# Kernel tuning notes

Hardware: AMD Instinct MI355X
Metric: run time of the kernel (lower is better)

Reference implementation:

```python
import jax, jax.numpy as jnp
import numpy as np


@jax.custom_vjp
def binary_act(x):
    # sign forward, straight-through (clipped) backward, matching BinaryActivation
    return jnp.sign(x)

def _ba_fwd(x):
    return jnp.sign(x), x

def _ba_bwd(x, g):
    return (jnp.where((x >= -1.0) & (x <= 1.0), g, 0.0),)

binary_act.defvjp(_ba_fwd, _ba_bwd)


def conv2d(x, w, b, pad, groups):
    # x: NCHW, w: OIHW
    y = jax.lax.conv_general_dilated(
        x, w, window_strides=(1, 1), padding=[(pad, pad), (pad, pad)],
        feature_group_count=groups,
        dimension_numbers=("NCHW", "OIHW", "NCHW"))
    return y + b[None, :, None, None]


def bconv(x, w, b, pad, groups):
    # Binary_conv2d: weights and bias binarized via sign (no STE on weights in torch either)
    return conv2d(x, jnp.sign(w), jnp.sign(b), pad, groups)


def maxpool2(x):
    return jax.lax.reduce_window(x, -jnp.inf, jax.lax.max,
                                 (1, 1, 2, 2), (1, 1, 2, 2), "VALID")


def setup_inputs() -> dict:
    key = jax.random.key(0)
    ks = jax.random.split(key, 14)
    d = {}
    d["x"] = jax.random.normal(ks[0], (1024, 3, 32, 32), dtype=jnp.float32)
    # conv1: depthwise 3x3 (groups=3) then 1x1 3->128
    d["w1_dw"] = jax.random.normal(ks[1], (3, 1, 3, 3), dtype=jnp.float32) * 0.1
    d["b1_dw"] = jax.random.normal(ks[2], (3,), dtype=jnp.float32) * 0.1
    d["w1_pw"] = jax.random.normal(ks[3], (128, 3, 1, 1), dtype=jnp.float32) * 0.1
    d["b1_pw"] = jax.random.normal(ks[4], (128,), dtype=jnp.float32) * 0.1
    # conv2: depthwise 3x3 (groups=128) then 1x1 128->256
    d["w2_dw"] = jax.random.normal(ks[5], (128, 1, 3, 3), dtype=jnp.float32) * 0.1
    d["b2_dw"] = jax.random.normal(ks[6], (128,), dtype=jnp.float32) * 0.1
    d["w2_pw"] = jax.random.normal(ks[7], (256, 128, 1, 1), dtype=jnp.float32) * 0.1
    d["b2_pw"] = jax.random.normal(ks[8], (256,), dtype=jnp.float32) * 0.1
    # fc layers (full precision weights, sign applied to fc1 output only)
    d["fc1_w"] = jax.random.normal(ks[9], (1024, 256 * 8 * 8), dtype=jnp.float32) * (1.0 / np.sqrt(256 * 8 * 8))
    d["fc1_b"] = jnp.zeros((1024,), dtype=jnp.float32)
    d["fc2_w"] = jax.random.normal(ks[10], (10, 1024), dtype=jnp.float32) * (1.0 / np.sqrt(1024.0))
    d["fc2_b"] = jnp.zeros((10,), dtype=jnp.float32)
    return d


def reference(x, w1_dw, b1_dw, w1_pw, b1_pw, w2_dw, b2_dw, w2_pw, b2_pw,
              fc1_w, fc1_b, fc2_w, fc2_b):
    h = bconv(x, w1_dw, b1_dw, pad=1, groups=3)        # [B,3,32,32]
    h = bconv(h, w1_pw, b1_pw, pad=0, groups=1)        # [B,128,32,32]
    h = maxpool2(binary_act(h))                        # [B,128,16,16]
    h = bconv(h, w2_dw, b2_dw, pad=1, groups=128)      # [B,128,16,16]
    h = bconv(h, w2_pw, b2_pw, pad=0, groups=1)        # [B,256,16,16]
    h = maxpool2(binary_act(h))                        # [B,256,8,8]
    h = h.reshape(h.shape[0], -1)                      # [B,16384]
    h = binary_act(h @ fc1_w.T + fc1_b)                # [B,1024]
    return h @ fc2_w.T + fc2_b                         # [B,10]
```

## Files before the change

kernel.cpp:

```cpp
#include <hip/hip_runtime.h>


__device__ __forceinline__ int fsign(float v)  { return (v > 0.f) - (v < 0.f); }
__device__ __forceinline__ int dsign(double v) { return (v > 0.0) - (v < 0.0); }

typedef int v4i __attribute__((ext_vector_type(4)));

__device__ __forceinline__ void async16(const signed char* g, signed char* l) {
    __builtin_amdgcn_global_load_lds(
        (const __attribute__((address_space(1))) void*)g,
        (__attribute__((address_space(3))) void*)l, 16, 0, 0);
}

__global__ void k1_conv1(const float* __restrict__ x,
                         const float* __restrict__ w1dw, const float* __restrict__ b1dw,
                         const float* __restrict__ w1pw, const float* __restrict__ b1pw,
                         signed char* __restrict__ pooled1T)
{
    __shared__ float sdw[27], sbdw[3];
    __shared__ unsigned char spidx[128];
    int t = threadIdx.x;
    if (t < 27) sdw[t] = (float)fsign(w1dw[t]);
    if (t < 3)  sbdw[t] = (float)fsign(b1dw[t]);
    if (t < 128) {
        int b0 = w1pw[t * 3 + 0] > 0.f;
        int b1 = w1pw[t * 3 + 1] > 0.f;
        int b2 = w1pw[t * 3 + 2] > 0.f;
        int b3 = b1pw[t] > 0.f;
        spidx[t] = (unsigned char)(b0 | (b1 << 1) | (b2 << 2) | (b3 << 3));
    }
    __syncthreads();

    int g  = blockIdx.x * 256 + t;
    int px = g & 15, py = (g >> 4) & 15, n = g >> 8;

    double h[3][4];
    const float* xb = x + (size_t)n * 3 * 1024;
    #pragma unroll
    for (int c = 0; c < 3; c++) {
        const float* xc = xb + c * 1024;
        #pragma unroll
        for (int dy = 0; dy < 2; dy++)
        #pragma unroll
        for (int dx = 0; dx < 2; dx++) {
            int y = 2 * py + dy, xx = 2 * px + dx;
            double acc = (double)sbdw[c];
            #pragma unroll
            for (int ky = 0; ky < 3; ky++) {
                int yy = y + ky - 1;
                if (yy < 0 || yy > 31) continue;
                #pragma unroll
                for (int kx = 0; kx < 3; kx++) {
                    int xxx = xx + kx - 1;
                    if (xxx < 0 || xxx > 31) continue;
                    acc += (double)sdw[c * 9 + ky * 3 + kx] * (double)xc[yy * 32 + xxx];
                }
            }
            h[c][dy * 2 + dx] = acc;
        }
    }

    double tv[4][4];
    #pragma unroll
    for (int q = 0; q < 4; q++) {
        double u = h[0][q] + h[1][q];
        double v = h[0][q] - h[1][q];
        tv[0][q] = v - h[2][q];
        tv[1][q] = u - h[2][q];
        tv[2][q] = v + h[2][q];
        tv[3][q] = u + h[2][q];
    }
    int mpack = 0;
    #pragma unroll
    for (int bp = 0; bp < 4; bp++) {
        int mxP = -2, mnP = 2, mxM = -2, mnM = 2;
        #pragma unroll
        for (int q = 0; q < 4; q++) {
            int sP = dsign(tv[bp][q] + 1.0);
            int sM = dsign(tv[bp][q] - 1.0);
            mxP = max(mxP, sP); mnP = min(mnP, sP);
            mxM = max(mxM, sM); mnM = min(mnM, sM);
        }
        int pat1 = 1 | (bp << 1);
        int pat0 = (~pat1) & 7;
        mpack |= (mxP + 1)   << (2 * (pat1 | 8));
        mpack |= (mxM + 1)   << (2 * pat1);
        mpack |= ((-mnM) + 1) << (2 * (pat0 | 8));
        mpack |= ((-mnP) + 1) << (2 * pat0);
    }

    signed char* outb = pooled1T + (size_t)n * 32768 + (py * 16 + px) * 128;
    const int* pint = (const int*)spidx;
    for (int ob = 0; ob < 32; ob++) {
        int pw = pint[ob];
        int cur = 0;
        #pragma unroll
        for (int e = 0; e < 4; e++) {
            int pi = (pw >> (8 * e)) & 15;
            int mv = ((mpack >> (pi * 2)) & 3) - 1;
            cur |= (mv & 0xff) << (8 * e);
        }
        *(int*)(outb + ob * 4) = cur;
    }
}

__global__ void kprep2(const float* __restrict__ w2pw, const float* __restrict__ b2pw,
                       signed char* __restrict__ w2s, int* __restrict__ b2adj)
{
    int o = blockIdx.x * 64 + threadIdx.x;
    int rs = 0;
    for (int cq = 0; cq < 32; cq++) {
        float4 w = *(const float4*)(w2pw + (size_t)o * 128 + cq * 4);
        int s0 = fsign(w.x), s1 = fsign(w.y), s2 = fsign(w.z), s3 = fsign(w.w);
        rs += s0 + s1 + s2 + s3;
        int pk = (s0 & 0xff) | ((s1 & 0xff) << 8) | ((s2 & 0xff) << 16) | ((s3 & 0xff) << 24);
        *(int*)(w2s + (size_t)o * 128 + cq * 4) = pk;
    }
    b2adj[o] = fsign(b2pw[o]) - 32 * rs;
}

__global__ __launch_bounds__(256, 3) void k3_fused(
    const signed char* __restrict__ pooled1T,
    const float* __restrict__ w2dw, const float* __restrict__ b2dw,
    const signed char* __restrict__ w2s, const int* __restrict__ b2adj,
    signed char* __restrict__ hT2)
{
    __shared__ __align__(16) signed char Ps[32768];
    __shared__ __align__(16) signed char sw4[1152];
    __shared__ __align__(16) signed char sdb2[128];
    __shared__ int sb2adj[256];
    __shared__ __align__(16) signed char Os[64 * 80];

    int t = threadIdx.x, l = t & 63, wid = t >> 6;
    int n = blockIdx.x;
    const signed char* pb = pooled1T + (size_t)n * 32768;

    #pragma unroll
    for (int it = 0; it < 8; it++) {
        int off = it * 4096 + t * 16;
        int p = off >> 7, seg = (off >> 4) & 7;
        *(int4*)&Ps[p * 128 + ((seg ^ (p & 7)) * 16)] = *(const int4*)(pb + off);
    }
    for (int i = t; i < 1152; i += 256) {
        int c = i & 127, tap = i >> 7;
        sw4[tap * 128 + c] = (signed char)fsign(w2dw[c * 9 + tap]);
    }
    if (t < 128) sdb2[t] = (signed char)(fsign(b2dw[t]) + 1);
    if (t < 256) sb2adj[t] = b2adj[t];
    __syncthreads();

    int frow = l & 15;

    v4i af[4][2];
    #pragma unroll
    for (int ks = 0; ks < 2; ks++) {
        int c0 = ks * 64 + (l >> 4) * 16;
        int cc = c0 >> 4;
        int4 w4[9];
        #pragma unroll
        for (int tap = 0; tap < 9; tap++)
            w4[tap] = *(const int4*)&sw4[tap * 128 + c0];
        int4 sdbv = *(const int4*)&sdb2[c0];

        #pragma unroll
        for (int i = 0; i < 4; i++) {
            int r = (wid * 4 + i) * 16 + frow;
            int py = r >> 5, px2 = (r >> 2) & 7, dy = (r >> 1) & 1, dx = r & 1;
            int y = 2 * py + dy, x = 2 * px2 + dx;
            int4 cnt = (int4){0, 0, 0, 0};
            #pragma unroll
            for (int ky = 0; ky < 3; ky++) {
                int yy = y + ky - 1;
                int yc = min(max(yy, 0), 15);
                #pragma unroll
                for (int kx = 0; kx < 3; kx++) {
                    int xx2 = x + kx - 1;
                    int xc = min(max(xx2, 0), 15);
                    int inb = ((yy == yc) && (xx2 == xc)) ? 0x01010101 : 0;
                    int p = yc * 16 + xc;
                    int4 v = *(const int4*)&Ps[p * 128 + ((cc ^ (p & 7)) * 16)];
                    int4 w = w4[ky * 3 + kx];
                    cnt.x += ((v.x ^ w.x) >> 1) & inb;
                    cnt.y += ((v.y ^ w.y) >> 1) & inb;
                    cnt.z += ((v.z ^ w.z) >> 1) & inb;
                    cnt.w += ((v.w ^ w.w) >> 1) & inb;
                }
            }
            int valid = (1 + (y > 0) + (y < 15)) * (1 + (x > 0) + (x < 15));
            int mb = (valid + 31) * 0x01010101;
            int4 u;
            u.x = sdbv.x + mb - (cnt.x + cnt.x);
            u.y = sdbv.y + mb - (cnt.y + cnt.y);
            u.z = sdbv.z + mb - (cnt.z + cnt.z);
            u.w = sdbv.w + mb - (cnt.w + cnt.w);
            af[i][ks] = (v4i){u.x, u.y, u.z, u.w};
        }
    }

    for (int oc = 0; oc < 4; oc++) {
        v4i acc[4][4];
        #pragma unroll
        for (int i = 0; i < 4; i++)
            #pragma unroll
            for (int jt = 0; jt < 4; jt++) acc[i][jt] = (v4i){0, 0, 0, 0};

        #pragma unroll
        for (int ks = 0; ks < 2; ks++) {
            v4i bf[4];
            #pragma unroll
            for (int jt = 0; jt < 4; jt++)
                bf[jt] = *(const v4i*)(w2s + (size_t)(oc * 64 + jt * 16 + frow) * 128
                                       + ks * 64 + (l >> 4) * 16);
            #pragma unroll
            for (int i = 0; i < 4; i++)
                #pragma unroll
                for (int jt = 0; jt < 4; jt++)
                    acc[i][jt] = __builtin_amdgcn_mfma_i32_16x16x64_i8(af[i][ks], bf[jt], acc[i][jt], 0, 0, 0);
        }

        __syncthreads();
        #pragma unroll
        for (int jt = 0; jt < 4; jt++) {
            int o_l = jt * 16 + frow;
            int bia = sb2adj[oc * 64 + o_l];
            #pragma unroll
            for (int i = 0; i < 4; i++) {
                int mx = -2;
                #pragma unroll
                for (int rr = 0; rr < 4; rr++) {
                    int p = acc[i][jt][rr] + bia;
                    int s = (p > 0) - (p < 0);
                    mx = s > mx ? s : mx;
                }
                int pp = (wid * 4 + i) * 4 + (l >> 4);
                Os[o_l * 80 + pp] = (signed char)mx;
            }
        }
        __syncthreads();
        *(int4*)&hT2[(size_t)n * 16384 + oc * 4096 + t * 16]
            = *(const int4*)&Os[(t >> 2) * 80 + (t & 3) * 16];
    }
}

__global__ void kprep(const float* __restrict__ fc1w, signed char* __restrict__ BL)
{
    int t = threadIdx.x;
    int b = blockIdx.x;
    int j = b >> 4, kb = b & 15;
    int k0 = kb * 1024 + t * 4;
    float4 w = *(const float4*)(fc1w + (size_t)j * 16384 + k0);
    float we[4] = {w.x, w.y, w.z, w.w};
    int out[4] = {0, 0, 0, 0};
    #pragma unroll
    for (int e = 0; e < 4; e++) {
        int q = (int)rint((double)we[e] * 4294967296.0);
        q = min(max(q, -266338304), 266338304);
        int d0 = ((q + 64) & 127) - 64; q = (q - d0) >> 7;
        int d1 = ((q + 64) & 127) - 64; q = (q - d1) >> 7;
        int d2 = ((q + 64) & 127) - 64; q = (q - d2) >> 7;
        int d3 = q;
        out[0] |= (d0 & 0xff) << (8 * e);
        out[1] |= (d1 & 0xff) << (8 * e);
        out[2] |= (d2 & 0xff) << (8 * e);
        out[3] |= (d3 & 0xff) << (8 * e);
    }
    #pragma unroll
    for (int m = 0; m < 4; m++)
        *(int*)(BL + (size_t)(j * 4 + m) * 16384 + k0) = out[m];
}

__global__ __launch_bounds__(256, 2) void k4a_fc1(
    const signed char* __restrict__ hT2, const signed char* __restrict__ BL,
    double* __restrict__ Pd)
{
    __shared__ __align__(16) signed char smem[65536];
    int t = threadIdx.x, l = t & 63, wid = t >> 6;
    int nb0 = blockIdx.y * 128, jb0 = blockIdx.x * 128;
    int kh = blockIdx.z, k0 = kh * 8192;
    int wn0 = (wid >> 1) * 64, wj0 = (wid & 1) * 64;

    int srow = l >> 3;
    int sseg = ((l & 7) ^ srow) * 16;
    const signed char* gA = hT2 + (size_t)(nb0 + wid * 32 + srow) * 16384 + k0 + sseg;
    const signed char* gB = BL  + (size_t)(jb0 + wid * 32 + srow) * 16384 + k0 + sseg;

    v4i acc[4][4];
    #pragma unroll
    for (int i = 0; i < 4; i++)
        #pragma unroll
        for (int q = 0; q < 4; q++) acc[i][q] = (v4i){0, 0, 0, 0};

    {
        signed char* As = smem;
        signed char* Bs = smem + 16384;
        #pragma unroll
        for (int i = 0; i < 4; i++) {
            async16(gA + (size_t)i * 8 * 16384, As + (wid * 32 + i * 8) * 128);
            async16(gB + (size_t)i * 8 * 16384, Bs + (wid * 32 + i * 8) * 128);
        }
    }

    for (int it = 0; it < 64; it++) {
        __syncthreads();
        if (it + 1 < 64) {
            int kt = (it + 1) * 128;
            signed char* As = smem + ((it + 1) & 1) * 32768;
            signed char* Bs = As + 16384;
            #pragma unroll
            for (int i = 0; i < 4; i++) {
                async16(gA + (size_t)i * 8 * 16384 + kt, As + (wid * 32 + i * 8) * 128);
                async16(gB + (size_t)i * 8 * 16384 + kt, Bs + (wid * 32 + i * 8) * 128);
            }
        }
        const signed char* As = smem + (it & 1) * 32768;
        const signed char* Bs = As + 16384;
        #pragma unroll
        for (int ks = 0; ks < 2; ks++) {
            int sw = (((ks * 4) + (l >> 4)) ^ (l & 7)) * 16;
            v4i af[4], bf[4];
            #pragma unroll
            for (int i = 0; i < 4; i++)
                af[i] = *(const v4i*)&As[(wn0 + i * 16 + (l & 15)) * 128 + sw];
            #pragma unroll
            for (int q = 0; q < 4; q++)
                bf[q] = *(const v4i*)&Bs[(wj0 + q * 16 + (l & 15)) * 128 + sw];
            #pragma unroll
            for (int i = 0; i < 4; i++)
                #pragma unroll
                for (int q = 0; q < 4; q++)
                    acc[i][q] = __builtin_amdgcn_mfma_i32_16x16x64_i8(af[i], bf[q], acc[i][q], 0, 0, 0);
        }
    }

    __syncthreads();
    int* S = (int*)smem;
    #pragma unroll
    for (int i = 0; i < 4; i++)
        #pragma unroll
        for (int q = 0; q < 4; q++)
            #pragma unroll
            for (int rr = 0; rr < 4; rr++) {
                int n_l  = wn0 + i * 16 + (l >> 4) * 4 + rr;
                int jm_l = wj0 + q * 16 + (l & 15);
                S[n_l * 128 + jm_l] = acc[i][q][rr];
            }
    __syncthreads();

    #pragma unroll
    for (int e = 0; e < 16; e++) {
        int idx = t * 16 + e;
        int n_l = idx >> 5, j_l = idx & 31;
        int4 s = *(const int4*)&S[n_l * 128 + j_l * 4];
        double val = (double)s.x + 128.0 * (double)s.y
                   + 16384.0 * (double)s.z + 2097152.0 * (double)s.w;
        Pd[(size_t)kh * 1048576 + (size_t)(nb0 + n_l) * 1024 + blockIdx.x * 32 + j_l] = val;
    }
}

__global__ void k4b_comb(const double* __restrict__ Pd, const float* __restrict__ fc1b,
                         signed char* __restrict__ hs)
{
    int g = blockIdx.x * 256 + threadIdx.x;
    int n = g >> 8, j0 = (g & 255) * 4;
    const double SCALE = 1.0 / 4294967296.0;
    int outv = 0;
    #pragma unroll
    for (int e = 0; e < 4; e++) {
        int j = j0 + e;
        double v = Pd[(size_t)n * 1024 + j] + Pd[1048576 + (size_t)n * 1024 + j];
        double p = v * SCALE + (double)fc1b[j];
        outv |= (dsign(p) & 0xff) << (8 * e);
    }
    *(int*)(hs + (size_t)n * 1024 + j0) = outv;
}

__global__ __launch_bounds__(512) void k4_fc1_mfma(
    const signed char* __restrict__ hT2, const signed char* __restrict__ BL,
    const float* __restrict__ fc1b, signed char* __restrict__ hs)
{
    __shared__ __align__(16) signed char smem[65536];
    int t = threadIdx.x, l = t & 63, wid = t >> 6;
    int nb0 = blockIdx.y * 128, jb0 = blockIdx.x * 128;
    int wn0 = (wid >> 1) * 32;
    int wj0 = (wid & 1) * 64;

    int srow = l >> 3;
    int sseg = ((l & 7) ^ srow) * 16;
    const signed char* gA = hT2 + (size_t)(nb0 + wid * 16 + srow) * 16384 + sseg;
    const signed char* gB = BL  + (size_t)(jb0 + wid * 16 + srow) * 16384 + sseg;

    v4i acc[2][4];
    #pragma unroll
    for (int i = 0; i < 2; i++)
        #pragma unroll
        for (int q = 0; q < 4; q++) acc[i][q] = (v4i){0, 0, 0, 0};

    {
        signed char* As = smem;
        signed char* Bs = smem + 16384;
        #pragma unroll
        for (int i = 0; i < 2; i++) {
            async16(gA + (size_t)i * 8 * 16384, As + (wid * 16 + i * 8) * 128);
            async16(gB + (size_t)i * 8 * 16384, Bs + (wid * 16 + i * 8) * 128);
        }
    }

    for (int it = 0; it < 128; it++) {
        __syncthreads();
        if (it + 1 < 128) {
            int kt = (it + 1) * 128;
            signed char* As = smem + ((it + 1) & 1) * 32768;
            signed char* Bs = As + 16384;
            #pragma unroll
            for (int i = 0; i < 2; i++) {
                async16(gA + (size_t)i * 8 * 16384 + kt, As + (wid * 16 + i * 8) * 128);
                async16(gB + (size_t)i * 8 * 16384 + kt, Bs + (wid * 16 + i * 8) * 128);
            }
        }
        const signed char* As = smem + (it & 1) * 32768;
        const signed char* Bs = As + 16384;
        #pragma unroll
        for (int ks = 0; ks < 2; ks++) {
            int sw = (((ks * 4) + (l >> 4)) ^ (l & 7)) * 16;
            v4i af[2], bf[4];
            #pragma unroll
            for (int i = 0; i < 2; i++)
                af[i] = *(const v4i*)&As[(wn0 + i * 16 + (l & 15)) * 128 + sw];
            #pragma unroll
            for (int q = 0; q < 4; q++)
                bf[q] = *(const v4i*)&Bs[(wj0 + q * 16 + (l & 15)) * 128 + sw];
            #pragma unroll
            for (int i = 0; i < 2; i++)
                #pragma unroll
                for (int q = 0; q < 4; q++)
                    acc[i][q] = __builtin_amdgcn_mfma_i32_16x16x64_i8(af[i], bf[q], acc[i][q], 0, 0, 0);
        }
    }

    __syncthreads();
    int* S = (int*)smem;
    #pragma unroll
    for (int i = 0; i < 2; i++)
        #pragma unroll
        for (int q = 0; q < 4; q++)
            #pragma unroll
            for (int rr = 0; rr < 4; rr++) {
                int n_l  = wn0 + i * 16 + (l >> 4) * 4 + rr;
                int jm_l = wj0 + q * 16 + (l & 15);
                S[n_l * 128 + jm_l] = acc[i][q][rr];
            }
    __syncthreads();

    const double SCALE = 1.0 / 4294967296.0;
    #pragma unroll
    for (int i = 0; i < 8; i++) {
        int idx = t * 8 + i;
        int n_l = idx >> 5, j_l = idx & 31;
        int4 s = *(const int4*)&S[n_l * 128 + j_l * 4];
        double val = (double)s.x + 128.0 * (double)s.y
                   + 16384.0 * (double)s.z + 2097152.0 * (double)s.w;
        int j = blockIdx.x * 32 + j_l;
        double p = val * SCALE + (double)fc1b[j];
        hs[(size_t)(nb0 + n_l) * 1024 + j] = (signed char)((p > 0.0) - (p < 0.0));
    }
}

__global__ void k5_fc2(const signed char* __restrict__ hs,
                       const float* __restrict__ fc2w, const float* __restrict__ fc2b,
                       float* __restrict__ out)
{
    int idx = blockIdx.x * 64 + threadIdx.x;
    if (idx >= 10240) return;
    int n = idx / 10, m = idx - n * 10;
    const signed char* hr = hs + (size_t)n * 1024;
    const float* wr = fc2w + (size_t)m * 1024;
    double acc = (double)fc2b[m];
    for (int jb = 0; jb < 1024; jb += 16) {
        int4 hv = *(const int4*)(hr + jb);
        int wd[4] = {hv.x, hv.y, hv.z, hv.w};
        #pragma unroll
        for (int u = 0; u < 4; u++)
            #pragma unroll
            for (int e = 0; e < 4; e++)
                acc += (double)(signed char)(wd[u] >> (8 * e)) * (double)wr[jb + u * 4 + e];
    }
    out[idx] = (float)acc;
}

extern "C" void kernel_launch(void* const* d_in, const int* in_sizes, int n_in,
                              void* d_out, int out_size, void* d_ws, size_t ws_size,
                              hipStream_t stream)
{
    const float* x    = (const float*)d_in[0];
    const float* w1dw = (const float*)d_in[1];
    const float* b1dw = (const float*)d_in[2];
    const float* w1pw = (const float*)d_in[3];
    const float* b1pw = (const float*)d_in[4];
    const float* w2dw = (const float*)d_in[5];
    const float* b2dw = (const float*)d_in[6];
    const float* w2pw = (const float*)d_in[7];
    const float* b2pw = (const float*)d_in[8];
    const float* fc1w = (const float*)d_in[9];
    const float* fc1b = (const float*)d_in[10];
    const float* fc2w = (const float*)d_in[11];
    const float* fc2b = (const float*)d_in[12];
    float* out = (float*)d_out;

    char* ws = (char*)d_ws;
    signed char* pooled1T = (signed char*)(ws);
    signed char* hT2      = (signed char*)(ws + 67108864);
    signed char* w2s      = (signed char*)(ws + 83886080);
    int*         b2adj    = (int*)(ws + 83886080 + 32768);
    signed char* BL       = (signed char*)(ws);
    signed char* hs       = (signed char*)(ws + 83886080);
    double*      Pd       = (double*)(ws + 84934656);
    bool split = ws_size >= (size_t)84934656 + 16777216;

    hipLaunchKernelGGL(k1_conv1,  dim3(1024),  dim3(256), 0, stream,
                       x, w1dw, b1dw, w1pw, b1pw, pooled1T);
    hipLaunchKernelGGL(kprep2,    dim3(4),     dim3(64),  0, stream,
                       w2pw, b2pw, w2s, b2adj);
    hipLaunchKernelGGL(k3_fused,  dim3(1024),  dim3(256), 0, stream,
                       pooled1T, w2dw, b2dw, w2s, b2adj, hT2);
    hipLaunchKernelGGL(kprep,     dim3(16384), dim3(256), 0, stream,
                       fc1w, BL);
    if (split) {
        hipLaunchKernelGGL(k4a_fc1,  dim3(32, 8, 2), dim3(256), 0, stream,
                           hT2, BL, Pd);
        hipLaunchKernelGGL(k4b_comb, dim3(1024),     dim3(256), 0, stream,
                           Pd, fc1b, hs);
    } else {
        hipLaunchKernelGGL(k4_fc1_mfma, dim3(32, 8), dim3(512), 0, stream,
                           hT2, BL, fc1b, hs);
    }
    hipLaunchKernelGGL(k5_fc2,    dim3(160),   dim3(64),  0, stream,
                       hs, fc2w, fc2b, out);
}
```

Before: 320.2 us.

## Split fc1 K-loop across warp pairs and fuse sign-combine with fc2

The split-K fc1 MFMA kernel now runs 8 warps per block instead of 4. Each pair of warp groups handles one of the two 64-wide K sub-steps of every 128-byte tile, and the two partial accumulators are reduced through shared memory before writeout. This raises wave count per CU for latency hiding, at the cost of an extra reduction pass and more synchronisation. The combine kernel is also fused with fc2: each block computes the sign of fc1 for one row and reduces against fc2 weights in double, dropping a launch and the hs round trip.

```diff
diff --git a/kernel.cpp b/kernel.cpp
--- a/kernel.cpp
+++ b/kernel.cpp
@@ -269,7 +269,7 @@
         *(int*)(BL + (size_t)(j * 4 + m) * 16384 + k0) = out[m];
 }
 
-__global__ __launch_bounds__(256, 2) void k4a_fc1(
+__global__ __launch_bounds__(512, 4) void k4a_fc1(
     const signed char* __restrict__ hT2, const signed char* __restrict__ BL,
     double* __restrict__ Pd)
 {
@@ -277,12 +277,13 @@
     int t = threadIdx.x, l = t & 63, wid = t >> 6;
     int nb0 = blockIdx.y * 128, jb0 = blockIdx.x * 128;
     int kh = blockIdx.z, k0 = kh * 8192;
-    int wn0 = (wid >> 1) * 64, wj0 = (wid & 1) * 64;
+    int ksw = wid >> 2;
+    int wn0 = ((wid >> 1) & 1) * 64, wj0 = (wid & 1) * 64;
 
     int srow = l >> 3;
     int sseg = ((l & 7) ^ srow) * 16;
-    const signed char* gA = hT2 + (size_t)(nb0 + wid * 32 + srow) * 16384 + k0 + sseg;
-    const signed char* gB = BL  + (size_t)(jb0 + wid * 32 + srow) * 16384 + k0 + sseg;
+    const signed char* gA = hT2 + (size_t)(nb0 + wid * 16 + srow) * 16384 + k0 + sseg;
+    const signed char* gB = BL  + (size_t)(jb0 + wid * 16 + srow) * 16384 + k0 + sseg;
 
     v4i acc[4][4];
     #pragma unroll
@@ -294,11 +295,13 @@
         signed char* As = smem;
         signed char* Bs = smem + 16384;
         #pragma unroll
-        for (int i = 0; i < 4; i++) {
-            async16(gA + (size_t)i * 8 * 16384, As + (wid * 32 + i * 8) * 128);
-            async16(gB + (size_t)i * 8 * 16384, Bs + (wid * 32 + i * 8) * 128);
-        }
-    }
+        for (int c = 0; c < 2; c++) {
+            async16(gA + (size_t)c * 8 * 16384, As + (wid * 16 + c * 8) * 128);
+            async16(gB + (size_t)c * 8 * 16384, Bs + (wid * 16 + c * 8) * 128);
+        }
+    }
+
+    int sw = (((ksw * 4) + (l >> 4)) ^ (l & 7)) * 16;
 
     for (int it = 0; it < 64; it++) {
         __syncthreads();
@@ -307,48 +310,59 @@
             signed char* As = smem + ((it + 1) & 1) * 32768;
             signed char* Bs = As + 16384;
             #pragma unroll
-            for (int i = 0; i < 4; i++) {
-                async16(gA + (size_t)i * 8 * 16384 + kt, As + (wid * 32 + i * 8) * 128);
-                async16(gB + (size_t)i * 8 * 16384 + kt, Bs + (wid * 32 + i * 8) * 128);
+            for (int c = 0; c < 2; c++) {
+                async16(gA + (size_t)c * 8 * 16384 + kt, As + (wid * 16 + c * 8) * 128);
+                async16(gB + (size_t)c * 8 * 16384 + kt, Bs + (wid * 16 + c * 8) * 128);
             }
         }
         const signed char* As = smem + (it & 1) * 32768;
         const signed char* Bs = As + 16384;
-        #pragma unroll
-        for (int ks = 0; ks < 2; ks++) {
-            int sw = (((ks * 4) + (l >> 4)) ^ (l & 7)) * 16;
-            v4i af[4], bf[4];
-            #pragma unroll
-            for (int i = 0; i < 4; i++)
-                af[i] = *(const v4i*)&As[(wn0 + i * 16 + (l & 15)) * 128 + sw];
+        v4i af[4], bf[4];
+        #pragma unroll
+        for (int i = 0; i < 4; i++)
+            af[i] = *(const v4i*)&As[(wn0 + i * 16 + (l & 15)) * 128 + sw];
+        #pragma unroll
+        for (int q = 0; q < 4; q++)
+            bf[q] = *(const v4i*)&Bs[(wj0 + q * 16 + (l & 15)) * 128 + sw];
+        #pragma unroll
+        for (int i = 0; i < 4; i++)
             #pragma unroll
             for (int q = 0; q < 4; q++)
-                bf[q] = *(const v4i*)&Bs[(wj0 + q * 16 + (l & 15)) * 128 + sw];
-            #pragma unroll
-            for (int i = 0; i < 4; i++)
-                #pragma unroll
-                for (int q = 0; q < 4; q++)
-                    acc[i][q] = __builtin_amdgcn_mfma_i32_16x16x64_i8(af[i], bf[q], acc[i][q], 0, 0, 0);
-        }
+                acc[i][q] = __builtin_amdgcn_mfma_i32_16x16x64_i8(af[i], bf[q], acc[i][q], 0, 0, 0);
     }
 
     __syncthreads();
     int* S = (int*)smem;
-    #pragma unroll
-    for (int i = 0; i < 4; i++)
-        #pragma unroll
-        for (int q = 0; q < 4; q++)
-            #pragma unroll
-            for (int rr = 0; rr < 4; rr++) {
-                int n_l  = wn0 + i * 16 + (l >> 4) * 4 + rr;
-                int jm_l = wj0 + q * 16 + (l & 15);
-                S[n_l * 128 + jm_l] = acc[i][q][rr];
-            }
-    __syncthreads();
-
-    #pragma unroll
-    for (int e = 0; e < 16; e++) {
-        int idx = t * 16 + e;
+    if (ksw == 0) {
+        #pragma unroll
+        for (int i = 0; i < 4; i++)
+            #pragma unroll
+            for (int q = 0; q < 4; q++)
+                #pragma unroll
+                for (int rr = 0; rr < 4; rr++) {
+                    int n_l  = wn0 + i * 16 + (l >> 4) * 4 + rr;
+                    int jm_l = wj0 + q * 16 + (l & 15);
+                    S[n_l * 128 + jm_l] = acc[i][q][rr];
+                }
+    }
+    __syncthreads();
+    if (ksw == 1) {
+        #pragma unroll
+        for (int i = 0; i < 4; i++)
+            #pragma unroll
+            for (int q = 0; q < 4; q++)
+                #pragma unroll
+                for (int rr = 0; rr < 4; rr++) {
+                    int n_l  = wn0 + i * 16 + (l >> 4) * 4 + rr;
+                    int jm_l = wj0 + q * 16 + (l & 15);
+                    S[n_l * 128 + jm_l] += acc[i][q][rr];
+                }
+    }
+    __syncthreads();
+
+    #pragma unroll
+    for (int e = 0; e < 8; e++) {
+        int idx = t * 8 + e;
         int n_l = idx >> 5, j_l = idx & 31;
         int4 s = *(const int4*)&S[n_l * 128 + j_l * 4];
         double val = (double)s.x + 128.0 * (double)s.y
@@ -357,21 +371,44 @@
     }
 }
 
-__global__ void k4b_comb(const double* __restrict__ Pd, const float* __restrict__ fc1b,
-                         signed char* __restrict__ hs)
-{
-    int g = blockIdx.x * 256 + threadIdx.x;
-    int n = g >> 8, j0 = (g & 255) * 4;
+__global__ __launch_bounds__(256) void k45_comb_fc2(
+    const double* __restrict__ Pd, const float* __restrict__ fc1b,
+    const float* __restrict__ fc2w, const float* __restrict__ fc2b,
+    float* __restrict__ out)
+{
+    __shared__ double sj[1024];
+    __shared__ double pw[4][10];
+    int t = threadIdx.x, n = blockIdx.x;
     const double SCALE = 1.0 / 4294967296.0;
-    int outv = 0;
-    #pragma unroll
-    for (int e = 0; e < 4; e++) {
-        int j = j0 + e;
+
+    #pragma unroll
+    for (int rep = 0; rep < 4; rep++) {
+        int j = rep * 256 + t;
         double v = Pd[(size_t)n * 1024 + j] + Pd[1048576 + (size_t)n * 1024 + j];
         double p = v * SCALE + (double)fc1b[j];
-        outv |= (dsign(p) & 0xff) << (8 * e);
-    }
-    *(int*)(hs + (size_t)n * 1024 + j0) = outv;
+        sj[j] = (double)((p > 0.0) - (p < 0.0));
+    }
+    __syncthreads();
+
+    int j0 = t * 4;
+    double s0 = sj[j0], s1 = sj[j0 + 1], s2 = sj[j0 + 2], s3 = sj[j0 + 3];
+    double acc[10];
+    #pragma unroll
+    for (int m = 0; m < 10; m++) {
+        float4 w = *(const float4*)(fc2w + (size_t)m * 1024 + j0);
+        acc[m] = s0 * (double)w.x + s1 * (double)w.y + s2 * (double)w.z + s3 * (double)w.w;
+    }
+    #pragma unroll
+    for (int off = 32; off > 0; off >>= 1)
+        #pragma unroll
+        for (int m = 0; m < 10; m++)
+            acc[m] += __shfl_down(acc[m], off);
+    if ((t & 63) == 0)
+        #pragma unroll
+        for (int m = 0; m < 10; m++) pw[t >> 6][m] = acc[m];
+    __syncthreads();
+    if (t < 10)
+        out[n * 10 + t] = (float)(pw[0][t] + pw[1][t] + pw[2][t] + pw[3][t] + (double)fc2b[t]);
 }
 
 __global__ __launch_bounds__(512) void k4_fc1_mfma(
@@ -525,14 +562,14 @@
     hipLaunchKernelGGL(kprep,     dim3(16384), dim3(256), 0, stream,
                        fc1w, BL);
     if (split) {
-        hipLaunchKernelGGL(k4a_fc1,  dim3(32, 8, 2), dim3(256), 0, stream,
+        hipLaunchKernelGGL(k4a_fc1,      dim3(32, 8, 2), dim3(512), 0, stream,
                            hT2, BL, Pd);
-        hipLaunchKernelGGL(k4b_comb, dim3(1024),     dim3(256), 0, stream,
-                           Pd, fc1b, hs);
+        hipLaunchKernelGGL(k45_comb_fc2, dim3(1024),     dim3(256), 0, stream,
+                           Pd, fc1b, fc2w, fc2b, out);
     } else {
         hipLaunchKernelGGL(k4_fc1_mfma, dim3(32, 8), dim3(512), 0, stream,
                            hT2, BL, fc1b, hs);
-    }
-    hipLaunchKernelGGL(k5_fc2,    dim3(160),   dim3(64),  0, stream,
-                       hs, fc2w, fc2b, out);
-}
+        hipLaunchKernelGGL(k5_fc2,      dim3(160),   dim3(64),  0, stream,
+                           hs, fc2w, fc2b, out);
+    }
+}
```

Result: faster. 298.3 us (-6.8%).
